# Performance work log

Measured on AMD Instinct MI355X. Metric: run time of the kernel, lower is better.

Reference implementation:

```python
import jax, jax.numpy as jnp
import numpy as np

B, L, H, NL, NRES = 64, 2048, 64, 10, 3
EPS = 1e-5


def _conv1d(x, w, b, pad):
    # x: [B, C, L], w: [O, I, K] (torch layout)
    y = jax.lax.conv_general_dilated(x, w, window_strides=(1,), padding=[(pad, pad)],
                                     dimension_numbers=("NCH", "OIH", "NCH"))
    return y + b[None, :, None]


def _bn(x, g, b, m, v):
    # eval-mode BatchNorm1d over channel dim of [B, C, L]
    scale = (g * jax.lax.rsqrt(v + EPS))[None, :, None]
    return (x - m[None, :, None]) * scale + b[None, :, None]


def _lstm_layer(x, w_ih, w_hh, b_ih, b_hh):
    # x: [T, B, H]; gate order (torch): i, f, g, o
    gates_x = jnp.einsum("tbh,gh->tbg", x, w_ih) + (b_ih + b_hh)  # [T, B, 4H]

    def step(carry, gx):
        h, c = carry
        gates = gx + h @ w_hh.T
        i, f, g, o = jnp.split(gates, 4, axis=-1)
        c = jax.nn.sigmoid(f) * c + jax.nn.sigmoid(i) * jnp.tanh(g)
        h = jax.nn.sigmoid(o) * jnp.tanh(c)
        return (h, c), h

    nb = x.shape[1]
    init = (jnp.zeros((nb, H), x.dtype), jnp.zeros((nb, H), x.dtype))
    _, hs = jax.lax.scan(step, init, gates_x)
    return hs  # [T, B, H]


def setup_inputs() -> dict:
    key = jax.random.key(0)
    ks = jax.random.split(key, 24)
    r = lambda i, shape, s=0.05: jax.random.normal(ks[i], shape, jnp.float32) * s
    inp = {
        "input": jax.random.normal(ks[0], (B, L, 4), jnp.float32),
        "mc": jax.random.uniform(ks[1], (B,), dtype=jnp.float32),
        "conv1_w": r(2, (32, 4, 1), 0.3), "conv1_b": r(3, (32,)),
        "conv2_w": r(4, (64, 32, 1), 0.2), "conv2_b": r(5, (64,)),
        "res_bn1_g": jnp.ones((NRES, 64), jnp.float32), "res_bn1_b": jnp.zeros((NRES, 64), jnp.float32),
        "res_bn1_m": jnp.zeros((NRES, 64), jnp.float32), "res_bn1_v": jnp.ones((NRES, 64), jnp.float32),
        "res_conv1_w": r(6, (NRES, 64, 64, 11)), "res_conv1_b": r(7, (NRES, 64)),
        "res_bn2_g": jnp.ones((NRES, 64), jnp.float32), "res_bn2_b": jnp.zeros((NRES, 64), jnp.float32),
        "res_bn2_m": jnp.zeros((NRES, 64), jnp.float32), "res_bn2_v": jnp.ones((NRES, 64), jnp.float32),
        "res_conv2_w": r(8, (NRES, 64, 64, 11)), "res_conv2_b": r(9, (NRES, 64)),
        "lstm_w_ih": r(10, (NL, 4 * H, H), 0.1), "lstm_w_hh": r(11, (NL, 4 * H, H), 0.1),
        "lstm_b_ih": r(12, (NL, 4 * H)), "lstm_b_hh": r(13, (NL, 4 * H)),
        "out_w": r(14, (H, 2), 0.1), "out_b": r(15, (2,)),
        "l": L,
    }
    return inp


def reference(input, mc, conv1_w, conv1_b, conv2_w, conv2_b,
              res_bn1_g, res_bn1_b, res_bn1_m, res_bn1_v, res_conv1_w, res_conv1_b,
              res_bn2_g, res_bn2_b, res_bn2_m, res_bn2_v, res_conv2_w, res_conv2_b,
              lstm_w_ih, lstm_w_hh, lstm_b_ih, lstm_b_hh, out_w, out_b, l):
    # mc and l are computed/accepted but never used by the original forward.
    x = jnp.transpose(input, (0, 2, 1))                    # [B, 4, L]
    x = jax.nn.relu(_conv1d(x, conv1_w, conv1_b, 0))       # [B, 32, L]
    x = jax.nn.relu(_conv1d(x, conv2_w, conv2_b, 0))       # [B, 64, L]
    for i in range(NRES):                                  # 3 pre-activation residual units
        h = jax.nn.relu(_bn(x, res_bn1_g[i], res_bn1_b[i], res_bn1_m[i], res_bn1_v[i]))
        h = _conv1d(h, res_conv1_w[i], res_conv1_b[i], 5)
        h = jax.nn.relu(_bn(h, res_bn2_g[i], res_bn2_b[i], res_bn2_m[i], res_bn2_v[i]))
        h = _conv1d(h, res_conv2_w[i], res_conv2_b[i], 5)
        x = x + h
    x = jnp.transpose(x, (2, 0, 1))                        # [L, B, 64] (seq-first, like torch LSTM)
    for layer in range(NL):
        x = _lstm_layer(x, lstm_w_ih[layer], lstm_w_hh[layer], lstm_b_ih[layer], lstm_b_hh[layer])
    logits = x[-1] @ out_w + out_b                         # [B, 2]
    return jax.nn.log_softmax(logits, axis=1)
```

## Files before the change

kernel.cpp:

```cpp
#include <hip/hip_runtime.h>
#include <hip/hip_bf16.h>

#define TL 2048
#define NB 64
#define NH 64
#define NLAY 10
#define NRESU 3
#define RSTEP 64

typedef float f32x4 __attribute__((ext_vector_type(4)));
typedef unsigned u32x2 __attribute__((ext_vector_type(2)));
typedef short bhalf8 __attribute__((ext_vector_type(8)));

__device__ __forceinline__ unsigned short f2bf(float f) {
    unsigned u = __float_as_uint(f);
    unsigned r = u + 0x7fffu + ((u >> 16) & 1u);
    return (unsigned short)(r >> 16);
}
__device__ __forceinline__ float bf2f(unsigned short h) {
    return __uint_as_float(((unsigned)h) << 16);
}
__device__ __forceinline__ float fast_sigmoid(float x) {
    return __builtin_amdgcn_rcpf(1.0f + __expf(-x));
}
__device__ __forceinline__ float fast_tanh(float x) {
    float e = __expf(2.0f * x);
    return 1.0f - 2.0f * __builtin_amdgcn_rcpf(e + 1.0f);
}

__global__ __launch_bounds__(256) void k_frontend(
    const float* __restrict__ in,
    const float* __restrict__ c1w, const float* __restrict__ c1b,
    const float* __restrict__ c2w, const float* __restrict__ c2b,
    float* __restrict__ x0)
{
    __shared__ float s_c1w[128];
    __shared__ float s_c1b[32];
    __shared__ float s_c2w[64 * 33];
    __shared__ float s_c2b[64];
    __shared__ float h1[64 * 33];
    __shared__ float ot[64 * 65];
    int tid = threadIdx.x;
    int b = blockIdx.x >> 5;
    int l0 = (blockIdx.x & 31) << 6;
    if (tid < 128) s_c1w[tid] = c1w[tid];
    if (tid < 32) s_c1b[tid] = c1b[tid];
    if (tid < 64) s_c2b[tid] = c2b[tid];
    for (int r = tid; r < 2048; r += 256) s_c2w[(r >> 5) * 33 + (r & 31)] = c2w[r];
    __syncthreads();
    if (tid < 64) {
        const float* ip = in + ((size_t)b * TL + l0 + tid) * 4;
        float x0v = ip[0], x1 = ip[1], x2 = ip[2], x3 = ip[3];
#pragma unroll
        for (int o = 0; o < 32; o++) {
            float a = s_c1w[o * 4 + 0] * x0v + s_c1w[o * 4 + 1] * x1 +
                      s_c1w[o * 4 + 2] * x2 + s_c1w[o * 4 + 3] * x3 + s_c1b[o];
            h1[tid * 33 + o] = fmaxf(a, 0.0f);
        }
    }
    __syncthreads();
    {
        int o = tid & 63, lg = tid >> 6;
#pragma unroll
        for (int j = 0; j < 16; j++) {
            int l = lg * 16 + j;
            float a = s_c2b[o];
#pragma unroll
            for (int i = 0; i < 32; i++) a += h1[l * 33 + i] * s_c2w[o * 33 + i];
            ot[o * 65 + l] = fmaxf(a, 0.0f);
        }
    }
    __syncthreads();
    for (int r = 0; r < 16; r++) {
        int idx = tid + 256 * r;
        int c = idx >> 6, l = idx & 63;
        x0[((size_t)b * 64 + c) * TL + l0 + l] = ot[c * 65 + l];
    }
}

__global__ __launch_bounds__(256) void k_prepw(const float* __restrict__ w, float* __restrict__ wt)
{
    int idx = blockIdx.x * 256 + threadIdx.x;
    if (idx >= NRESU * 64 * 64 * 11) return;
    int k = idx % 11;
    int rest = idx / 11;
    int i = rest & 63;
    int o = (rest >> 6) & 63;
    int uu = rest >> 12;
    wt[(((size_t)uu * 64 + i) * 11 + k) * 64 + o] = w[idx];
}

__global__ __launch_bounds__(256) void k_resconv(
    const float* __restrict__ in, float* __restrict__ out,
    const float* __restrict__ wt, const float* __restrict__ bias,
    const float* __restrict__ bg, const float* __restrict__ bb,
    const float* __restrict__ bm, const float* __restrict__ bv,
    int accumulate)
{
    __shared__ float sscale[64], sshift[64];
    __shared__ float ht[64 * 139];
    int tid = threadIdx.x;
    int b = blockIdx.x >> 4;
    int l0 = (blockIdx.x & 15) << 7;
    if (tid < 64) {
        float sc = bg[tid] * rsqrtf(bv[tid] + 1e-5f);
        sscale[tid] = sc;
        sshift[tid] = bb[tid] - bm[tid] * sc;
    }
    __syncthreads();
    for (int r = 0; r < 35; r++) {
        int idx = tid + 256 * r;
        if (idx < 64 * 138) {
            int i = idx / 138, ll = idx - i * 138;
            int l = l0 - 5 + ll;
            float v = 0.0f;
            if (l >= 0 && l < TL) v = in[((size_t)b * 64 + i) * TL + l];
            ht[i * 139 + ll] = fmaxf(v * sscale[i] + sshift[i], 0.0f);
        }
    }
    __syncthreads();
    int o = tid & 63, lq = tid >> 6;
    float acc[32];
#pragma unroll
    for (int j = 0; j < 32; j++) acc[j] = 0.0f;
    for (int i = 0; i < 64; i++) {
        float wr[11];
#pragma unroll
        for (int k = 0; k < 11; k++) wr[k] = wt[(i * 11 + k) * 64 + o];
        float hr[42];
        const float* hp = ht + i * 139 + lq * 32;
#pragma unroll
        for (int k = 0; k < 42; k++) hr[k] = hp[k];
#pragma unroll
        for (int k = 0; k < 11; k++)
#pragma unroll
            for (int j = 0; j < 32; j++) acc[j] += hr[k + j] * wr[k];
    }
    float bsv = bias[o];
    float* op = out + ((size_t)b * 64 + o) * TL + l0 + lq * 32;
    if (accumulate) {
#pragma unroll
        for (int j = 0; j < 32; j++) op[j] += acc[j] + bsv;
    } else {
#pragma unroll
        for (int j = 0; j < 32; j++) op[j] = acc[j] + bsv;
    }
}

__global__ __launch_bounds__(256) void k_transpose(
    const float* __restrict__ x0, unsigned short* __restrict__ Xbf)
{
    __shared__ float t[64 * 65];
    int tid = threadIdx.x;
    int b = blockIdx.x >> 5;
    int t0 = (blockIdx.x & 31) << 6;
    for (int r = 0; r < 16; r++) {
        int idx = tid + 256 * r;
        int c = idx >> 6, tt = idx & 63;
        t[c * 65 + tt] = x0[((size_t)b * 64 + c) * TL + t0 + tt];
    }
    __syncthreads();
    for (int r = 0; r < 16; r++) {
        int idx = tid + 256 * r;
        int tt = idx >> 6, c = idx & 63;
        Xbf[((size_t)(t0 + tt)) * (NB * NH) + b * 64 + c] = f2bf(t[c * 65 + tt]);
    }
}

__global__ __launch_bounds__(512) void k_lstm(
    const unsigned short* __restrict__ Xbf,
    const float* __restrict__ w_ih, const float* __restrict__ w_hh,
    const float* __restrict__ b_ih, const float* __restrict__ b_hh,
    unsigned short* __restrict__ ring, float* __restrict__ final_h, int* prog)
{
    int bid = blockIdx.x;
    int grp = bid & 7;
    int layer = bid >> 3;
    if (grp >= 4 || layer >= NLAY) return;
    int b0 = grp * 16;
    int tid = threadIdx.x;
    int w = tid >> 6;
    int lane = tid & 63;
    int l15 = lane & 15, l4 = lane >> 4;
    int self = layer * 4 + grp;
    const bool has_store = (layer < NLAY - 1);
    const bool use_ring = (layer > 0);
    int brow = tid >> 5;
    int cc0 = (tid & 31) * 2;
    int T0 = w * 2, T1 = w * 2 + 1;

    __shared__ __align__(16) unsigned short XH[2][16][136];
    __shared__ float gbuf[16][16][17];

    bhalf8 Bh[2][4];
#pragma unroll
    for (int s = 0; s < 2; s++) {
        int n = (w * 2 + s) * 16 + l15;
        const float* rih = w_ih + ((size_t)layer * 256 + n) * 64;
        const float* rhh = w_hh + ((size_t)layer * 256 + n) * 64;
#pragma unroll
        for (int kt = 0; kt < 4; kt++) {
#pragma unroll
            for (int j = 0; j < 8; j++) {
                int k = kt * 32 + l4 * 8 + j;
                float v = (k < 64) ? rih[k] : rhh[k - 64];
                Bh[s][kt][j] = (short)f2bf(v);
            }
        }
    }
    float bv[8];
#pragma unroll
    for (int g = 0; g < 4; g++) {
#pragma unroll
        for (int s = 0; s < 2; s++) {
            int n = g * 64 + cc0 + s;
            bv[g * 2 + s] = b_ih[layer * 256 + n] + b_hh[layer * 256 + n];
        }
    }
    for (int idx = tid; idx < 2 * 16 * 64; idx += 512) {
        XH[idx >> 10][(idx >> 6) & 15][64 + (idx & 63)] = 0;
    }
    float cst[2] = {0.f, 0.f};

    int* p_self = prog + self * 32;
    int* p_prev = prog + (self - 4) * 32;
    int* p_next = prog + (self + 4) * 32;
    int cached_prev = 0, cached_next = 0;

#define POLL_GE(ptr, tgt, cachev)                                                     \
    if (cachev < (tgt)) {                                                             \
        int v_; long g_ = 0;                                                          \
        while ((v_ = __hip_atomic_load(ptr, __ATOMIC_ACQUIRE,                         \
                        __HIP_MEMORY_SCOPE_AGENT)) < (tgt) && ++g_ < 1500000)         \
            __builtin_amdgcn_s_sleep(2);                                              \
        cachev = v_;                                                                  \
    }

    if (tid == 0 && layer > 0) { POLL_GE(p_prev, 32, cached_prev); }
    __syncthreads();
    unsigned px[4];
    {
        unsigned p0;
        if (!use_ring) {
            const unsigned short* s0 = Xbf + (size_t)(b0 + brow) * 64 + cc0;
            asm volatile("global_load_dword %0, %1, off" : "=&v"(p0) : "v"(s0) : "memory");
        } else {
            const unsigned short* s0 = ring + ((size_t)(layer - 1) * RSTEP) * 4096 + (b0 + brow) * 64 + cc0;
            asm volatile("global_load_dword %0, %1, off sc0 sc1" : "=&v"(p0) : "v"(s0) : "memory");
        }
        asm volatile("s_waitcnt vmcnt(0)" ::: "memory");
        __builtin_amdgcn_sched_barrier(0);
        *(unsigned*)&XH[0][brow][cc0] = p0;
#pragma unroll
        for (int pre = 1; pre <= 3; pre++) {
            if (!use_ring) {
                const unsigned short* sp = Xbf + ((size_t)pre * NB + b0 + brow) * 64 + cc0;
                asm volatile("global_load_dword %0, %1, off" : "=&v"(px[pre]) : "v"(sp) : "memory");
            } else {
                const unsigned short* sp = ring + ((size_t)(layer - 1) * RSTEP + pre) * 4096 + (b0 + brow) * 64 + cc0;
                asm volatile("global_load_dword %0, %1, off sc0 sc1" : "=&v"(px[pre]) : "v"(sp) : "memory");
            }
        }
    }
    asm volatile("s_waitcnt vmcnt(0)" ::: "memory");
    __builtin_amdgcn_sched_barrier(0);
    __syncthreads();

    for (int t0 = 0; t0 < TL; t0 += 8) {
#pragma unroll
        for (int ts = 0; ts < 8; ++ts) {
            const int p = ts & 1, q = p ^ 1;
            const int t = t0 + ts;
            const int cons = (ts + 1) & 3;
            const int pref = ts & 3;

            f32x4 Acc0 = {0, 0, 0, 0}, Acc1 = {0, 0, 0, 0};
#pragma unroll
            for (int kt = 0; kt < 4; kt++) {
                bhalf8 Ah = *(const bhalf8*)&XH[p][l15][kt * 32 + l4 * 8];
                Acc0 = __builtin_amdgcn_mfma_f32_16x16x32_bf16(Ah, Bh[0][kt], Acc0, 0, 0, 0);
                Acc1 = __builtin_amdgcn_mfma_f32_16x16x32_bf16(Ah, Bh[1][kt], Acc1, 0, 0, 0);
            }
#pragma unroll
            for (int r = 0; r < 4; r++) {
                gbuf[T0][l4 * 4 + r][l15] = Acc0[r];
                gbuf[T1][l4 * 4 + r][l15] = Acc1[r];
            }
            asm volatile("s_waitcnt lgkmcnt(0)" ::: "memory");
            __builtin_amdgcn_s_barrier();
            __builtin_amdgcn_sched_barrier(0);

            if (has_store) { asm volatile("s_waitcnt vmcnt(4)" ::: "memory"); }
            else           { asm volatile("s_waitcnt vmcnt(2)" ::: "memory"); }
            __builtin_amdgcn_sched_barrier(0);

            *(unsigned*)&XH[q][brow][cc0] = px[cons];

            int tb = cc0 >> 4, cb = cc0 & 15;
            float hv[2];
#pragma unroll
            for (int s = 0; s < 2; s++) {
                float gi = gbuf[0 * 4 + tb][brow][cb + s] + bv[0 + s];
                float gf = gbuf[1 * 4 + tb][brow][cb + s] + bv[2 + s];
                float gg = gbuf[2 * 4 + tb][brow][cb + s] + bv[4 + s];
                float go = gbuf[3 * 4 + tb][brow][cb + s] + bv[6 + s];
                float c = fast_sigmoid(gf) * cst[s] + fast_sigmoid(gi) * fast_tanh(gg);
                cst[s] = c;
                hv[s] = fast_sigmoid(go) * fast_tanh(c);
            }
            unsigned hw = ((unsigned)f2bf(hv[1]) << 16) | (unsigned)f2bf(hv[0]);

            *(unsigned*)&XH[q][brow][64 + cc0] = hw;
            if (has_store) {
                unsigned short* ap = ring + ((size_t)layer * RSTEP + (t & 63)) * 4096 + (b0 + brow) * 64 + cc0;
                asm volatile("global_store_dword %0, %1, off sc0 sc1" :: "v"(ap), "v"(hw) : "memory");
            } else if (t == TL - 1) {
                final_h[(b0 + brow) * NH + cc0] = hv[0];
                final_h[(b0 + brow) * NH + cc0 + 1] = hv[1];
            }

            {
                int tt = t + 4; if (tt > TL - 1) tt = TL - 1;
                if (!use_ring) {
                    const unsigned short* sp = Xbf + ((size_t)tt * NB + b0 + brow) * 64 + cc0;
                    asm volatile("global_load_dword %0, %1, off" : "=&v"(px[pref]) : "v"(sp) : "memory");
                } else {
                    const unsigned short* sp = ring + ((size_t)(layer - 1) * RSTEP + (tt & 63)) * 4096 + (b0 + brow) * 64 + cc0;
                    asm volatile("global_load_dword %0, %1, off sc0 sc1" : "=&v"(px[pref]) : "v"(sp) : "memory");
                }
            }

            asm volatile("s_waitcnt lgkmcnt(0)" ::: "memory");
            __builtin_amdgcn_s_barrier();
            __builtin_amdgcn_sched_barrier(0);
        }

        if (has_store) { asm volatile("s_waitcnt vmcnt(1)" ::: "memory"); }
        __builtin_amdgcn_s_barrier();
        __builtin_amdgcn_sched_barrier(0);
        if (tid == 0) {
            __hip_atomic_store(p_self, t0, __ATOMIC_RELEASE, __HIP_MEMORY_SCOPE_AGENT);
            int nt0 = t0 + 8;
            if (nt0 < TL) {
                if (use_ring) {
                    int tgt = nt0 + 16; if (tgt > TL) tgt = TL;
                    POLL_GE(p_prev, tgt, cached_prev);
                }
                if (has_store) {
                    int need = nt0 - 64;
                    if (need > 0) { POLL_GE(p_next, need, cached_next); }
                }
            }
        }
        __builtin_amdgcn_s_barrier();
        __builtin_amdgcn_sched_barrier(0);
    }

    asm volatile("s_waitcnt vmcnt(0)" ::: "memory");
    __builtin_amdgcn_s_barrier();
    if (tid == 0) {
        __hip_atomic_store(p_self, TL, __ATOMIC_RELEASE, __HIP_MEMORY_SCOPE_AGENT);
    }
#undef POLL_GE
}

__global__ void k_head(const float* __restrict__ fh, const float* __restrict__ ow,
                       const float* __restrict__ ob, float* __restrict__ out)
{
    int b = threadIdx.x;
    if (b >= NB) return;
    const float* h = fh + b * NH;
    float l0 = ob[0], l1 = ob[1];
    for (int uu = 0; uu < 64; uu++) { l0 += h[uu] * ow[uu * 2]; l1 += h[uu] * ow[uu * 2 + 1]; }
    float m = fmaxf(l0, l1);
    float s = expf(l0 - m) + expf(l1 - m);
    float ls = m + logf(s);
    out[b * 2] = l0 - ls;
    out[b * 2 + 1] = l1 - ls;
}

extern "C" void kernel_launch(void* const* d_in, const int* in_sizes, int n_in,
                              void* d_out, int out_size, void* d_ws, size_t ws_size,
                              hipStream_t stream) {
    const float* input = (const float*)d_in[0];
    const float* c1w = (const float*)d_in[2];
    const float* c1b = (const float*)d_in[3];
    const float* c2w = (const float*)d_in[4];
    const float* c2b = (const float*)d_in[5];
    const float* bn1g = (const float*)d_in[6];
    const float* bn1b = (const float*)d_in[7];
    const float* bn1m = (const float*)d_in[8];
    const float* bn1v = (const float*)d_in[9];
    const float* rw1 = (const float*)d_in[10];
    const float* rb1 = (const float*)d_in[11];
    const float* bn2g = (const float*)d_in[12];
    const float* bn2b = (const float*)d_in[13];
    const float* bn2m = (const float*)d_in[14];
    const float* bn2v = (const float*)d_in[15];
    const float* rw2 = (const float*)d_in[16];
    const float* rb2 = (const float*)d_in[17];
    const float* wih = (const float*)d_in[18];
    const float* whh = (const float*)d_in[19];
    const float* bih = (const float*)d_in[20];
    const float* bhh = (const float*)d_in[21];
    const float* outw = (const float*)d_in[22];
    const float* outb = (const float*)d_in[23];

    float* ws = (float*)d_ws;
    float*          x0buf = ws;
    float*          t1buf = x0buf + 8388608;
    unsigned short* Xbf   = (unsigned short*)(t1buf + 8388608);
    unsigned short* ringb = Xbf + 8388608;
    float*          fhbuf = (float*)(ringb + 2359296);
    int*            progb = (int*)(fhbuf + 4096);
    float*          wt1   = (float*)(progb + 40 * 32);
    float*          wt2   = wt1 + NRESU * 64 * 64 * 11;

    hipMemsetAsync(progb, 0, 40 * 32 * sizeof(int), stream);

    k_prepw<<<528, 256, 0, stream>>>(rw1, wt1);
    k_prepw<<<528, 256, 0, stream>>>(rw2, wt2);
    k_frontend<<<2048, 256, 0, stream>>>(input, c1w, c1b, c2w, c2b, x0buf);
    for (int uu = 0; uu < NRESU; uu++) {
        k_resconv<<<1024, 256, 0, stream>>>(x0buf, t1buf, wt1 + uu * 45056, rb1 + uu * 64,
                                            bn1g + uu * 64, bn1b + uu * 64, bn1m + uu * 64, bn1v + uu * 64, 0);
        k_resconv<<<1024, 256, 0, stream>>>(t1buf, x0buf, wt2 + uu * 45056, rb2 + uu * 64,
                                            bn2g + uu * 64, bn2b + uu * 64, bn2m + uu * 64, bn2v + uu * 64, 1);
    }
    k_transpose<<<2048, 256, 0, stream>>>(x0buf, Xbf);
    k_lstm<<<80, 512, 0, stream>>>(Xbf, wih, whh, bih, bhh, ringb, fhbuf, progb);
    k_head<<<1, 64, 0, stream>>>(fhbuf, outw, outb, (float*)d_out);
}
```

Measured before the change: 3.089 ms.

## Use bf16 split-precision MFMA for residual convolutions

Rewrites the residual conv kernel to run on 16x16x32 bf16 matrix instructions instead of scalar FP32 FMAs. Activations and weights are each split into bf16 high and low parts, and three MFMA products are summed to approximate FP32 accuracy. A new weight-prep kernel produces the split bf16 weights in a k-major, output-by-input layout, and results are staged through shared memory for coalesced stores. It costs three times the matrix ops and a small loss of precision compared with full FP32.

```diff
diff --git a/kernel.cpp b/kernel.cpp
--- a/kernel.cpp
+++ b/kernel.cpp
@@ -78,72 +78,122 @@
     }
 }
 
-__global__ __launch_bounds__(256) void k_prepw(const float* __restrict__ w, float* __restrict__ wt)
+__global__ __launch_bounds__(256) void k_prepw_mfma(
+    const float* __restrict__ w, unsigned short* __restrict__ wbh, unsigned short* __restrict__ wbl)
 {
     int idx = blockIdx.x * 256 + threadIdx.x;
-    if (idx >= NRESU * 64 * 64 * 11) return;
-    int k = idx % 11;
-    int rest = idx / 11;
-    int i = rest & 63;
-    int o = (rest >> 6) & 63;
-    int uu = rest >> 12;
-    wt[(((size_t)uu * 64 + i) * 11 + k) * 64 + o] = w[idx];
-}
-
-__global__ __launch_bounds__(256) void k_resconv(
+    if (idx >= NRESU * 11 * 64 * 64) return;
+    int i = idx & 63;
+    int rest = idx >> 6;
+    int o = rest & 63;
+    rest >>= 6;
+    int k = rest % 11;
+    int u = rest / 11;
+    float v = w[(((size_t)u * 64 + o) * 64 + i) * 11 + k];
+    unsigned short hb = f2bf(v);
+    float lo = v - bf2f(hb);
+    wbh[idx] = hb;
+    wbl[idx] = f2bf(lo);
+}
+
+__global__ __launch_bounds__(256) void k_resconv_mfma(
     const float* __restrict__ in, float* __restrict__ out,
-    const float* __restrict__ wt, const float* __restrict__ bias,
+    const unsigned short* __restrict__ wbh, const unsigned short* __restrict__ wbl,
+    const float* __restrict__ bias,
     const float* __restrict__ bg, const float* __restrict__ bb,
     const float* __restrict__ bm, const float* __restrict__ bv,
     int accumulate)
 {
     __shared__ float sscale[64], sshift[64];
-    __shared__ float ht[64 * 139];
+    __shared__ __align__(16) char smem[41472];
+    unsigned short* XTH = (unsigned short*)smem;
+    unsigned short* XTL = XTH + 144 * 72;
+    float* Yb = (float*)smem;
+
     int tid = threadIdx.x;
     int b = blockIdx.x >> 4;
     int l0 = (blockIdx.x & 15) << 7;
+    int lane = tid & 63;
+    int wv = tid >> 6;
+    int l15 = lane & 15, l4 = lane >> 4;
+
     if (tid < 64) {
         float sc = bg[tid] * rsqrtf(bv[tid] + 1e-5f);
         sscale[tid] = sc;
         sshift[tid] = bb[tid] - bm[tid] * sc;
     }
     __syncthreads();
-    for (int r = 0; r < 35; r++) {
-        int idx = tid + 256 * r;
-        if (idx < 64 * 138) {
-            int i = idx / 138, ll = idx - i * 138;
+
+    {
+        int i = tid >> 2, ll0 = (tid & 3) * 36;
+        float sc = sscale[i], sh = sshift[i];
+        const float* ip = in + ((size_t)b * 64 + i) * TL;
+#pragma unroll
+        for (int j = 0; j < 36; j++) {
+            int ll = ll0 + j;
             int l = l0 - 5 + ll;
             float v = 0.0f;
-            if (l >= 0 && l < TL) v = in[((size_t)b * 64 + i) * TL + l];
-            ht[i * 139 + ll] = fmaxf(v * sscale[i] + sshift[i], 0.0f);
-        }
-    }
-    __syncthreads();
-    int o = tid & 63, lq = tid >> 6;
-    float acc[32];
-#pragma unroll
-    for (int j = 0; j < 32; j++) acc[j] = 0.0f;
-    for (int i = 0; i < 64; i++) {
-        float wr[11];
-#pragma unroll
-        for (int k = 0; k < 11; k++) wr[k] = wt[(i * 11 + k) * 64 + o];
-        float hr[42];
-        const float* hp = ht + i * 139 + lq * 32;
-#pragma unroll
-        for (int k = 0; k < 42; k++) hr[k] = hp[k];
-#pragma unroll
-        for (int k = 0; k < 11; k++)
-#pragma unroll
-            for (int j = 0; j < 32; j++) acc[j] += hr[k + j] * wr[k];
-    }
-    float bsv = bias[o];
-    float* op = out + ((size_t)b * 64 + o) * TL + l0 + lq * 32;
-    if (accumulate) {
-#pragma unroll
-        for (int j = 0; j < 32; j++) op[j] += acc[j] + bsv;
-    } else {
-#pragma unroll
-        for (int j = 0; j < 32; j++) op[j] = acc[j] + bsv;
+            if (l >= 0 && l < TL) v = fmaxf(ip[l] * sc + sh, 0.0f);
+            unsigned short hb = f2bf(v);
+            float lo = v - bf2f(hb);
+            XTH[ll * 72 + i] = hb;
+            XTL[ll * 72 + i] = f2bf(lo);
+        }
+    }
+    __syncthreads();
+
+    f32x4 acc[2][4];
+#pragma unroll
+    for (int s = 0; s < 2; s++)
+#pragma unroll
+        for (int ot = 0; ot < 4; ot++) acc[s][ot] = (f32x4){0, 0, 0, 0};
+
+    for (int k = 0; k < 11; k++) {
+#pragma unroll
+        for (int ic = 0; ic < 2; ic++) {
+            bhalf8 ah[2], al[2];
+#pragma unroll
+            for (int s = 0; s < 2; s++) {
+                int row = (wv * 2 + s) * 16 + l15 + k;
+                ah[s] = *(const bhalf8*)&XTH[row * 72 + ic * 32 + l4 * 8];
+                al[s] = *(const bhalf8*)&XTL[row * 72 + ic * 32 + l4 * 8];
+            }
+#pragma unroll
+            for (int ot = 0; ot < 4; ot++) {
+                size_t woff = ((size_t)(k * 64 + ot * 16 + l15)) * 64 + ic * 32 + l4 * 8;
+                bhalf8 bh = *(const bhalf8*)&wbh[woff];
+                bhalf8 bl = *(const bhalf8*)&wbl[woff];
+#pragma unroll
+                for (int s = 0; s < 2; s++) {
+                    acc[s][ot] = __builtin_amdgcn_mfma_f32_16x16x32_bf16(ah[s], bh, acc[s][ot], 0, 0, 0);
+                    acc[s][ot] = __builtin_amdgcn_mfma_f32_16x16x32_bf16(al[s], bh, acc[s][ot], 0, 0, 0);
+                    acc[s][ot] = __builtin_amdgcn_mfma_f32_16x16x32_bf16(ah[s], bl, acc[s][ot], 0, 0, 0);
+                }
+            }
+        }
+    }
+    __syncthreads();
+
+#pragma unroll
+    for (int s = 0; s < 2; s++)
+#pragma unroll
+        for (int ot = 0; ot < 4; ot++)
+#pragma unroll
+            for (int r = 0; r < 4; r++)
+                Yb[((wv * 2 + s) * 16 + l4 * 4 + r) * 66 + ot * 16 + l15] = acc[s][ot][r];
+    __syncthreads();
+
+    {
+        int o = tid >> 2, ls0 = (tid & 3) * 32;
+        float bsv = bias[o];
+        float* op = out + ((size_t)b * 64 + o) * TL + l0 + ls0;
+        if (accumulate) {
+#pragma unroll
+            for (int j = 0; j < 32; j++) op[j] += Yb[(ls0 + j) * 66 + o] + bsv;
+        } else {
+#pragma unroll
+            for (int j = 0; j < 32; j++) op[j] = Yb[(ls0 + j) * 66 + o] + bsv;
+        }
     }
 }
 
@@ -413,19 +463,23 @@
     unsigned short* ringb = Xbf + 8388608;
     float*          fhbuf = (float*)(ringb + 2359296);
     int*            progb = (int*)(fhbuf + 4096);
-    float*          wt1   = (float*)(progb + 40 * 32);
-    float*          wt2   = wt1 + NRESU * 64 * 64 * 11;
+    unsigned short* wbh1  = (unsigned short*)(progb + 40 * 32);
+    unsigned short* wbl1  = wbh1 + NRESU * 11 * 64 * 64;
+    unsigned short* wbh2  = wbl1 + NRESU * 11 * 64 * 64;
+    unsigned short* wbl2  = wbh2 + NRESU * 11 * 64 * 64;
 
     hipMemsetAsync(progb, 0, 40 * 32 * sizeof(int), stream);
 
-    k_prepw<<<528, 256, 0, stream>>>(rw1, wt1);
-    k_prepw<<<528, 256, 0, stream>>>(rw2, wt2);
+    k_prepw_mfma<<<528, 256, 0, stream>>>(rw1, wbh1, wbl1);
+    k_prepw_mfma<<<528, 256, 0, stream>>>(rw2, wbh2, wbl2);
     k_frontend<<<2048, 256, 0, stream>>>(input, c1w, c1b, c2w, c2b, x0buf);
     for (int uu = 0; uu < NRESU; uu++) {
-        k_resconv<<<1024, 256, 0, stream>>>(x0buf, t1buf, wt1 + uu * 45056, rb1 + uu * 64,
-                                            bn1g + uu * 64, bn1b + uu * 64, bn1m + uu * 64, bn1v + uu * 64, 0);
-        k_resconv<<<1024, 256, 0, stream>>>(t1buf, x0buf, wt2 + uu * 45056, rb2 + uu * 64,
-                                            bn2g + uu * 64, bn2b + uu * 64, bn2m + uu * 64, bn2v + uu * 64, 1);
+        k_resconv_mfma<<<1024, 256, 0, stream>>>(x0buf, t1buf, wbh1 + uu * 45056, wbl1 + uu * 45056,
+                                                 rb1 + uu * 64, bn1g + uu * 64, bn1b + uu * 64,
+                                                 bn1m + uu * 64, bn1v + uu * 64, 0);
+        k_resconv_mfma<<<1024, 256, 0, stream>>>(t1buf, x0buf, wbh2 + uu * 45056, wbl2 + uu * 45056,
+                                                 rb2 + uu * 64, bn2g + uu * 64, bn2b + uu * 64,
+                                                 bn2m + uu * 64, bn2v + uu * 64, 1);
     }
     k_transpose<<<2048, 256, 0, stream>>>(x0buf, Xbf);
     k_lstm<<<80, 512, 0, stream>>>(Xbf, wih, whh, bih, bhh, ringb, fhbuf, progb);
```

Measured after the change: 2.832 ms. 1.09x faster.
